# Performance work log

Measured on AMD Instinct MI355X. Metric: run time of the kernel, lower is better.

Reference implementation:

```python
import jax, jax.numpy as jnp
from jax import lax
import numpy as np

B, T = 64, 50
N_POINTS, N_STATE, N_ACTION = 3, 6, 2
ROWS = COLS = 64          # local env window
RES = 0.03                # meters / pixel
PADDING = 200
H_FULL = W_FULL = 256
FC = 256
C_IN = N_POINTS + 1 + N_ACTION  # rope channels + local env + action smear
FLAT = 32 * 14 * 14


def setup_inputs() -> dict:
    key = jax.random.key(0)
    ks = jax.random.split(key, 10)
    action = jax.random.normal(ks[0], (B, T, N_ACTION), jnp.float32) * 0.1
    state = jax.random.normal(ks[1], (B, T + 1, N_STATE), jnp.float32) * 0.3
    res = jnp.full((B, T, 1), RES, jnp.float32)
    full_env = (jax.random.uniform(ks[2], (B, H_FULL, W_FULL)) > 0.9).astype(jnp.float32)
    full_env_origin = jnp.full((B, 2), H_FULL / 2, jnp.float32)
    conv_w1 = jax.random.normal(ks[3], (3, 3, C_IN, 16), jnp.float32) * 0.1
    conv_b1 = jnp.zeros((16,), jnp.float32)
    conv_w2 = jax.random.normal(ks[4], (3, 3, 16, 32), jnp.float32) * 0.1
    conv_b2 = jnp.zeros((32,), jnp.float32)
    d_in = N_STATE + N_ACTION + FLAT
    dense_w0 = jax.random.normal(ks[5], (d_in, FC), jnp.float32) * 0.01
    dense_b0 = jnp.zeros((FC,), jnp.float32)
    dense_w1 = jax.random.normal(ks[6], (FC, FC), jnp.float32) * 0.01
    dense_b1 = jnp.zeros((FC,), jnp.float32)
    dense_w2 = jax.random.normal(ks[7], (FC, N_STATE), jnp.float32) * 0.01
    dense_b2 = jnp.zeros((N_STATE,), jnp.float32)
    return dict(action=action, state=state, res=res, full_env=full_env,
                full_env_origin=full_env_origin,
                conv_w1=conv_w1, conv_b1=conv_b1, conv_w2=conv_w2, conv_b2=conv_b2,
                dense_w0=dense_w0, dense_b0=dense_b0, dense_w1=dense_w1,
                dense_b1=dense_b1, dense_w2=dense_w2, dense_b2=dense_b2)


def _forward(action, state, res, full_env, full_env_origin,
             conv_w1, conv_b1, conv_w2, conv_b2,
             dense_w0, dense_b0, dense_w1, dense_b1, dense_w2, dense_b2):
    s0 = state[:, 0]                     # [B, N_STATE]
    res0 = res[:, 0, 0]                  # [B]
    origin = full_env_origin             # [B, 2] (row, col) pixel origin
    padded = jnp.pad(full_env, ((0, 0), (PADDING, PADDING), (PADDING, PADDING)))
    bi = jnp.arange(B)
    dr = jnp.arange(-(ROWS // 2), ROWS // 2)
    dc = jnp.arange(-(COLS // 2), COLS // 2)
    half = jnp.array([ROWS // 2, COLS // 2], jnp.float32)
    pi = jnp.arange(N_POINTS)[None, :]

    def raster(points, local_origin):
        # points [B, P, 2] (x, y) meters; local_origin [B, 2] (row, col)
        r = (points[..., 1] / res0[:, None] + local_origin[:, 0:1]).astype(jnp.int32)
        c = (points[..., 0] / res0[:, None] + local_origin[:, 1:2]).astype(jnp.int32)
        valid = (r >= 0) & (r < ROWS) & (c >= 0) & (c < COLS)
        rc = jnp.clip(r, 0, ROWS - 1)
        cc = jnp.clip(c, 0, COLS - 1)
        img = jnp.zeros((B, ROWS, COLS, N_POINTS), jnp.float32)
        img = img.at[bi[:, None], rc, cc, pi].add(valid.astype(jnp.float32))
        return jnp.minimum(img, 1.0)

    def step(s_t, a_t):
        head = s_t[:, -2:]                                   # (x, y) of head point
        ccol = (head[:, 0] / RES + origin[:, 1]).astype(jnp.int32)
        crow = (head[:, 1] / RES + origin[:, 0]).astype(jnp.int32)
        ri = crow[:, None, None] + dr[None, :, None] + PADDING   # [B, ROWS, COLS]
        ci = ccol[:, None, None] + dc[None, None, :] + PADDING
        local = padded[bi[:, None, None], ri, ci]                # gather local window
        local_origin = origin - jnp.stack([crow, ccol], 1).astype(jnp.float32) + half
        rope_img = raster(s_t.reshape(B, N_POINTS, 2), local_origin)
        act_img = jnp.broadcast_to(a_t[:, None, None, :], (B, ROWS, COLS, N_ACTION))
        z = jnp.concatenate([rope_img, local[..., None], act_img], axis=-1)
        for w, b in ((conv_w1, conv_b1), (conv_w2, conv_b2)):
            z = jax.nn.relu(lax.conv_general_dilated(
                z, w, (1, 1), 'VALID',
                dimension_numbers=('NHWC', 'HWIO', 'NHWC')) + b)
            z = lax.reduce_window(z, -jnp.inf, lax.max,
                                  (1, 2, 2, 1), (1, 2, 2, 1), 'VALID')
        z = z.reshape(B, -1)
        h = jnp.concatenate([s_t, a_t, z], axis=-1)              # mixed
        h = jax.nn.relu(h @ dense_w0 + dense_b0)
        h = jax.nn.relu(h @ dense_w1 + dense_b1)
        ds = h @ dense_w2 + dense_b2
        s_next = s_t + ds                                        # residual
        return s_next, s_next

    _, traj = lax.scan(step, s0, jnp.swapaxes(action, 0, 1))     # traj [T, B, N_STATE]
    return jnp.concatenate([s0[:, None], jnp.swapaxes(traj, 0, 1)], axis=1)


def reference(action, state, res, full_env, full_env_origin,
              conv_w1, conv_b1, conv_w2, conv_b2,
              dense_w0, dense_b0, dense_w1, dense_b1, dense_w2, dense_b2):
    return _forward(action, state, res, full_env, full_env_origin,
                    conv_w1, conv_b1, conv_w2, conv_b2,
                    dense_w0, dense_b0, dense_w1, dense_b1, dense_w2, dense_b2)
```

## Files before the change

kernel.cpp:

```cpp
#include <hip/hip_runtime.h>


__global__ __launch_bounds__(512)
void k_tail(const float* __restrict__ action, const float* __restrict__ w0,
            const float* __restrict__ b0, const float* __restrict__ w1d,
            const float* __restrict__ wsPart, const float* __restrict__ wsS,
            float* __restrict__ wsD1p, int st)
{
    const int b   = blockIdx.x >> 2;
    const int q   = blockIdx.x & 3;
    const int tid = threadIdx.x;

    __shared__ float hp[512];
    __shared__ float h1l[64];
    __shared__ float dp[512];

    const float* sp = wsS + ((st-1)&1)*512 + b*8;
    const float a0p = action[b*100 + (st-1)*2 + 0];
    const float a1p = action[b*100 + (st-1)*2 + 1];

    {
        const int cl  = tid & 63;
        const int ksg = tid >> 6;
        const int col = q*64 + cl;
        const float* pp = wsPart + b*8192 + ksg*4*256 + col;
        float h = pp[0] + pp[256] + pp[512] + pp[768];
        if (ksg == 0){
            h += b0[col];
            #pragma unroll
            for (int j = 0; j < 6; j++) h = fmaf(sp[j], w0[j*256 + col], h);
            h = fmaf(a0p, w0[1536 + col], h);
            h = fmaf(a1p, w0[1792 + col], h);
        }
        hp[tid] = h;
    }
    __syncthreads();
    if (tid < 64){
        float s = hp[tid]       + hp[64 + tid]  + hp[128 + tid] + hp[192 + tid]
                + hp[256 + tid] + hp[320 + tid] + hp[384 + tid] + hp[448 + tid];
        h1l[tid] = fmaxf(s, 0.f);
    }
    __syncthreads();

    {
        const int colp = tid & 255;
        const int kh   = tid >> 8;
        const float* wrow = w1d + (q*64 + kh*32)*256 + colp;
        const float* hh   = h1l + kh*32;
        float d0 = 0.f, d1 = 0.f;
        #pragma unroll 8
        for (int k = 0; k < 32; k += 2){
            d0 = fmaf(hh[k],   wrow[k*256],     d0);
            d1 = fmaf(hh[k+1], wrow[(k+1)*256], d1);
        }
        dp[tid] = d0 + d1;
    }
    __syncthreads();
    if (tid < 256)
        wsD1p[b*1024 + q*256 + tid] = dp[tid] + dp[256 + tid];
}

__device__ inline void tail_finish(int b, int tid, int st,
                                   const float* __restrict__ wsD1p,
                                   const float* __restrict__ b1d,
                                   const float* __restrict__ w2d,
                                   const float* __restrict__ b2d,
                                   const float* __restrict__ wsS,
                                   float* __restrict__ wred,
                                   float* __restrict__ sSl)
{
    const float* dd = wsD1p + b*1024 + tid;
    float h2 = fmaxf(dd[0] + dd[256] + dd[512] + dd[768] + b1d[tid], 0.f);
    float p[6];
    const float* wr = w2d + tid*6;
    #pragma unroll
    for (int j = 0; j < 6; j++) p[j] = h2 * wr[j];
    #pragma unroll
    for (int off = 32; off > 0; off >>= 1){
        #pragma unroll
        for (int j = 0; j < 6; j++) p[j] += __shfl_down(p[j], off, 64);
    }
    if ((tid & 63) == 0){
        #pragma unroll
        for (int j = 0; j < 6; j++) wred[(tid >> 6)*6 + j] = p[j];
    }
    __syncthreads();
    if (tid < 6){
        float ds = wred[tid] + wred[6+tid] + wred[12+tid] + wred[18+tid] + b2d[tid];
        sSl[tid] = wsS[((st-1)&1)*512 + b*8 + tid] + ds;
    }
    __syncthreads();
}

__global__ __launch_bounds__(256, 2)
void k_conv(const float* __restrict__ action, const float* __restrict__ state,
            const float* __restrict__ res, const float* __restrict__ env,
            const float* __restrict__ origin,
            const float* __restrict__ w1, const float* __restrict__ b1,
            const float* __restrict__ w2, const float* __restrict__ b2,
            const float* __restrict__ b1d, const float* __restrict__ w2d,
            const float* __restrict__ b2d, const float* __restrict__ wsD1p,
            float* __restrict__ wsS, float* __restrict__ wsFlatT,
            float* __restrict__ out, int st)
{
    const int wg  = blockIdx.x;
    const int b   = wg >> 3;
    const int oct = wg & 7;
    const int tid = threadIdx.x;

    __shared__ float w1l[864];
    __shared__ float w2l[4608];
    __shared__ float b2l[32];
    __shared__ float bAl[16];
    __shared__ float sSl[8];
    __shared__ float wred[24];
    __shared__ int   prm[12];
    __shared__ float pool1s[6*31*20];
    __shared__ unsigned char inl[14*64];

    for (int i = tid; i < 216; i += 256)
        *(float4*)&w1l[i*4] = *(const float4*)(w1 + i*4);
    for (int i = tid; i < 1152; i += 256)
        *(float4*)&w2l[i*4] = *(const float4*)(w2 + i*4);
    if (tid < 32) b2l[tid] = b2[tid];

    if (st == 0){
        if (tid < 6) sSl[tid] = state[b*306 + tid];
        __syncthreads();
    } else {
        tail_finish(b, tid, st, wsD1p, b1d, w2d, b2d, wsS, wred, sSl);
    }

    if (oct == 0 && tid < 6){
        out[b*306 + st*6 + tid] = sSl[tid];
        wsS[(st & 1)*512 + b*8 + tid] = sSl[tid];
    }

    if (tid == 0){
        float org0 = origin[2*b], org1 = origin[2*b+1];
        int ccol = (int)(sSl[4] / 0.03f + org1);
        int crow = (int)(sSl[5] / 0.03f + org0);
        float res0 = res[b*50];
        float lo0 = org0 - (float)crow + 32.0f;
        float lo1 = org1 - (float)ccol + 32.0f;
        prm[0] = crow; prm[1] = ccol;
        #pragma unroll
        for (int p = 0; p < 3; p++){
            int rr = (int)(sSl[2*p+1]/res0 + lo0);
            int cc = (int)(sSl[2*p  ]/res0 + lo1);
            prm[2+p] = rr; prm[5+p] = cc;
            prm[8+p] = (rr>=0 && rr<64 && cc>=0 && cc<64) ? 1 : 0;
        }
    }
    if (tid < 16){
        float s4 = 0.f, s5 = 0.f;
        #pragma unroll
        for (int k = 0; k < 9; k++){
            s4 += w1[(k*6 + 4)*16 + tid];
            s5 += w1[(k*6 + 5)*16 + tid];
        }
        float a0 = action[b*100 + st*2 + 0];
        float a1 = action[b*100 + st*2 + 1];
        bAl[tid] = b1[tid] + a0*s4 + a1*s5;
    }
    __syncthreads();

    const int p2lo = (oct < 6) ? 2*oct : 12 + (oct - 6);
    const int p2n  = (oct < 6) ? 2 : 1;
    const int p1n  = 2*p2n + 2;
    const int p1lo = 2*p2lo;
    const int ilo  = 4*p2lo;
    const int inn  = 2*p1n + 2;

    {
        const int crow = prm[0], ccol = prm[1];
        for (int idx = tid; idx < inn*64; idx += 256){
            int i = idx >> 6, j = idx & 63;
            int r = crow - 32 + ilo + i;
            int c = ccol - 32 + j;
            float v = (r>=0 && r<256 && c>=0 && c<256) ? env[b*65536 + (r<<8) + c] : 0.f;
            inl[idx] = (unsigned char)v;
        }
    }
    __syncthreads();

    {
        int pr[3], pc[3], pvld[3];
        #pragma unroll
        for (int p = 0; p < 3; p++){ pr[p]=prm[2+p]; pc[p]=prm[5+p]; pvld[p]=prm[8+p]; }

        for (int u = tid; u < p1n*31; u += 256){
            int pl = u / 31;
            int j  = u - pl*31;
            float l[4][4];
            #pragma unroll
            for (int dy = 0; dy < 4; dy++)
                #pragma unroll
                for (int dx = 0; dx < 4; dx++)
                    l[dy][dx] = (float)inl[(2*pl + dy)*64 + 2*j + dx];

            float m[16];
            #pragma unroll
            for (int o = 0; o < 16; o++) m[o] = 0.f;

            #pragma unroll
            for (int dy = 0; dy < 2; dy++){
                #pragma unroll
                for (int dx = 0; dx < 2; dx++){
                    int rg = 2*(p1lo + pl) + dy;
                    int cg = 2*j + dx;
                    bool pf[3]; int pidx[3];
                    #pragma unroll
                    for (int p = 0; p < 3; p++){
                        int kr = pr[p] - rg, kc = pc[p] - cg;
                        pf[p] = pvld[p] && kr >= 0 && kr < 3 && kc >= 0 && kc < 3;
                        pidx[p] = pf[p] ? ((kr*3 + kc)*6 + p)*16 : 0;
                    }
                    #pragma unroll
                    for (int o = 0; o < 16; o++){
                        float v = bAl[o];
                        #pragma unroll
                        for (int kr = 0; kr < 3; kr++)
                            #pragma unroll
                            for (int kc = 0; kc < 3; kc++)
                                v = fmaf(l[dy+kr][dx+kc], w1l[((kr*3 + kc)*6 + 3)*16 + o], v);
                        if (pf[0]) v += w1l[pidx[0] + o];
                        if (pf[1]) v += w1l[pidx[1] + o];
                        if (pf[2]) v += w1l[pidx[2] + o];
                        v = fmaxf(v, 0.f);
                        m[o] = fmaxf(m[o], v);
                    }
                }
            }
            float* pd = &pool1s[(pl*31 + j)*20];
            *(float4*)(pd     ) = make_float4(m[0],  m[1],  m[2],  m[3]);
            *(float4*)(pd + 4 ) = make_float4(m[4],  m[5],  m[6],  m[7]);
            *(float4*)(pd + 8 ) = make_float4(m[8],  m[9],  m[10], m[11]);
            *(float4*)(pd + 12) = make_float4(m[12], m[13], m[14], m[15]);
        }
    }
    __syncthreads();

    for (int u = tid; u < p2n*14*8; u += 256){
        int pi  = u / 112;
        int rem = u - pi*112;
        int jj  = rem >> 3;
        int oq  = rem & 7;
        int o0  = oq*4;

        float acc[4][4];
        #pragma unroll
        for (int ps = 0; ps < 4; ps++)
            #pragma unroll
            for (int c = 0; c < 4; c++) acc[ps][c] = 0.f;

        #pragma unroll 1
        for (int t9 = 0; t9 < 9; t9++){
            int kr = t9 / 3, kc = t9 - 3*(t9/3);
            const float* pb = &pool1s[((2*pi + kr)*31 + (2*jj + kc))*20];
            const float* wb = &w2l[(kr*3 + kc)*512 + o0];
            #pragma unroll
            for (int kib = 0; kib < 4; kib++){
                float4 q00 = *(const float4*)(pb + kib*4);
                float4 q01 = *(const float4*)(pb + 20 + kib*4);
                float4 q10 = *(const float4*)(pb + 620 + kib*4);
                float4 q11 = *(const float4*)(pb + 640 + kib*4);
                float pq[4][4] = {
                    {q00.x, q00.y, q00.z, q00.w},
                    {q01.x, q01.y, q01.z, q01.w},
                    {q10.x, q10.y, q10.z, q10.w},
                    {q11.x, q11.y, q11.z, q11.w}};
                #pragma unroll
                for (int kk = 0; kk < 4; kk++){
                    float4 wv = *(const float4*)(wb + (kib*4 + kk)*32);
                    #pragma unroll
                    for (int ps = 0; ps < 4; ps++){
                        float pvv = pq[ps][kk];
                        acc[ps][0] = fmaf(pvv, wv.x, acc[ps][0]);
                        acc[ps][1] = fmaf(pvv, wv.y, acc[ps][1]);
                        acc[ps][2] = fmaf(pvv, wv.z, acc[ps][2]);
                        acc[ps][3] = fmaf(pvv, wv.w, acc[ps][3]);
                    }
                }
            }
        }
        int kb = ((p2lo + pi)*14 + jj)*32 + o0;
        #pragma unroll
        for (int c = 0; c < 4; c++){
            float bb = b2l[o0 + c];
            float v0 = fmaxf(acc[0][c] + bb, 0.f);
            float v1 = fmaxf(acc[1][c] + bb, 0.f);
            float v2 = fmaxf(acc[2][c] + bb, 0.f);
            float v3 = fmaxf(acc[3][c] + bb, 0.f);
            wsFlatT[(kb + c)*64 + b] = fmaxf(fmaxf(v0, v1), fmaxf(v2, v3));
        }
    }
}

__global__ __launch_bounds__(256, 2)
void k_dense0(const float* __restrict__ w0, const float* __restrict__ wsFlatT,
              float* __restrict__ wsPart)
{
    const int blk = blockIdx.x;
    const int lid = (blk & 7)*64 + (blk >> 3);
    const int ks = lid >> 4;
    const int nc = lid & 15;
    const int n0 = nc*16;
    const int tid  = threadIdx.x;
    const int w    = tid >> 6;
    const int lane = tid & 63;
    const int mg = lane >> 2;
    const int nq = lane & 3;
    const int kbase = ks*196;

    __shared__ float xs[196*68];

    for (int idx = tid; idx < 3136; idx += 256){
        int k  = idx >> 4;
        int b4 = idx & 15;
        float4 v = *(const float4*)(wsFlatT + (kbase + k)*64 + b4*4);
        *(float4*)(&xs[k*68 + b4*4]) = v;
    }
    __syncthreads();

    float acc[4][4];
    #pragma unroll
    for (int i = 0; i < 4; i++)
        #pragma unroll
        for (int c = 0; c < 4; c++) acc[i][c] = 0.f;

    const float* xk = xs + (49*w)*68 + mg*4;
    const float* wpp = w0 + (8 + kbase + 49*w)*256 + n0 + nq*4;
    #pragma unroll 7
    for (int k = 0; k < 49; k++){
        float4 x4 = *(const float4*)(xk + k*68);
        float4 w4 = *(const float4*)(wpp + k*256);
        acc[0][0]=fmaf(x4.x,w4.x,acc[0][0]); acc[0][1]=fmaf(x4.x,w4.y,acc[0][1]);
        acc[0][2]=fmaf(x4.x,w4.z,acc[0][2]); acc[0][3]=fmaf(x4.x,w4.w,acc[0][3]);
        acc[1][0]=fmaf(x4.y,w4.x,acc[1][0]); acc[1][1]=fmaf(x4.y,w4.y,acc[1][1]);
        acc[1][2]=fmaf(x4.y,w4.z,acc[1][2]); acc[1][3]=fmaf(x4.y,w4.w,acc[1][3]);
        acc[2][0]=fmaf(x4.z,w4.x,acc[2][0]); acc[2][1]=fmaf(x4.z,w4.y,acc[2][1]);
        acc[2][2]=fmaf(x4.z,w4.z,acc[2][2]); acc[2][3]=fmaf(x4.z,w4.w,acc[2][3]);
        acc[3][0]=fmaf(x4.w,w4.x,acc[3][0]); acc[3][1]=fmaf(x4.w,w4.y,acc[3][1]);
        acc[3][2]=fmaf(x4.w,w4.z,acc[3][2]); acc[3][3]=fmaf(x4.w,w4.w,acc[3][3]);
    }
    __syncthreads();

    float* red = xs;
    {
        float* rr = red + (w*64 + lane)*17;
        #pragma unroll
        for (int j = 0; j < 16; j++) rr[j] = acc[j>>2][j&3];
    }
    __syncthreads();
    if (tid < 64){
        int mg2 = tid >> 2, nq2 = tid & 3;
        #pragma unroll
        for (int g = 0; g < 4; g++){
            float4 v;
            v.x = red[tid*17+4*g+0] + red[(64+tid)*17+4*g+0] + red[(128+tid)*17+4*g+0] + red[(192+tid)*17+4*g+0];
            v.y = red[tid*17+4*g+1] + red[(64+tid)*17+4*g+1] + red[(128+tid)*17+4*g+1] + red[(192+tid)*17+4*g+1];
            v.z = red[tid*17+4*g+2] + red[(64+tid)*17+4*g+2] + red[(128+tid)*17+4*g+2] + red[(192+tid)*17+4*g+2];
            v.w = red[tid*17+4*g+3] + red[(64+tid)*17+4*g+3] + red[(128+tid)*17+4*g+3] + red[(192+tid)*17+4*g+3];
            int bb = mg2*4 + g;
            *(float4*)(wsPart + (bb*32 + ks)*256 + n0 + nq2*4) = v;
        }
    }
}

__global__ __launch_bounds__(256)
void k_fin(const float* __restrict__ b1d, const float* __restrict__ w2d,
           const float* __restrict__ b2d, const float* __restrict__ wsD1p,
           const float* __restrict__ wsS, float* __restrict__ out)
{
    const int b = blockIdx.x;
    const int tid = threadIdx.x;
    __shared__ float wred[24];
    __shared__ float sSl[8];
    tail_finish(b, tid, 50, wsD1p, b1d, w2d, b2d, wsS, wred, sSl);
    if (tid < 6) out[b*306 + 300 + tid] = sSl[tid];
}

extern "C" void kernel_launch(void* const* d_in, const int* in_sizes, int n_in,
                              void* d_out, int out_size, void* d_ws, size_t ws_size,
                              hipStream_t stream)
{
    (void)in_sizes; (void)n_in; (void)out_size; (void)ws_size;
    const float* action = (const float*)d_in[0];
    const float* state  = (const float*)d_in[1];
    const float* res    = (const float*)d_in[2];
    const float* env    = (const float*)d_in[3];
    const float* origin = (const float*)d_in[4];
    const float* w1  = (const float*)d_in[5];
    const float* b1  = (const float*)d_in[6];
    const float* w2  = (const float*)d_in[7];
    const float* b2  = (const float*)d_in[8];
    const float* w0  = (const float*)d_in[9];
    const float* b0  = (const float*)d_in[10];
    const float* w1d = (const float*)d_in[11];
    const float* b1d = (const float*)d_in[12];
    const float* w2d = (const float*)d_in[13];
    const float* b2d = (const float*)d_in[14];
    float* out = (float*)d_out;

    float* wsF     = (float*)d_ws;
    float* wsS     = wsF;
    float* wsD1p   = wsF + 1024;
    float* wsFlatT = wsF + 1024 + 65536;
    float* wsPart  = wsF + 1024 + 65536 + 401408;

    k_conv<<<dim3(512), dim3(256), 0, stream>>>(
        action, state, res, env, origin, w1, b1, w2, b2,
        b1d, w2d, b2d, wsD1p, wsS, wsFlatT, out, 0);
    k_dense0<<<dim3(512), dim3(256), 0, stream>>>(w0, wsFlatT, wsPart);

    for (int st = 1; st < 50; ++st){
        k_tail<<<dim3(256), dim3(512), 0, stream>>>(
            action, w0, b0, w1d, wsPart, wsS, wsD1p, st);
        k_conv<<<dim3(512), dim3(256), 0, stream>>>(
            action, state, res, env, origin, w1, b1, w2, b2,
            b1d, w2d, b2d, wsD1p, wsS, wsFlatT, out, st);
        k_dense0<<<dim3(512), dim3(256), 0, stream>>>(w0, wsFlatT, wsPart);
    }
    k_tail<<<dim3(256), dim3(512), 0, stream>>>(
        action, w0, b0, w1d, wsPart, wsS, wsD1p, 50);
    k_fin<<<dim3(64), dim3(256), 0, stream>>>(b1d, w2d, b2d, wsD1p, wsS, out);
}
```

Before: 1.811 ms.

## Split conv work by column halves, remap blocks per XCD, drop dense0 LDS staging

Each k_conv block now handles half of the output columns, which doubles the grid to 1024 blocks and shrinks the shared tiles. Occupancy bounds rise to 4 blocks per SM. Block indices in k_conv and k_tail are remapped so that all blocks for a given batch land on the same XCD, aiming for better L2 locality. k_dense0 now reads activations directly from global memory instead of staging them in LDS, removing one sync and the LDS footprint. The cost is that each column-half block reloads the weights, recomputes tail_finish, and computes its own halo columns, so some work is duplicated.

```diff
diff --git a/kernel.cpp b/kernel.cpp
--- a/kernel.cpp
+++ b/kernel.cpp
@@ -7,8 +7,10 @@
             const float* __restrict__ wsPart, const float* __restrict__ wsS,
             float* __restrict__ wsD1p, int st)
 {
-    const int b   = blockIdx.x >> 2;
-    const int q   = blockIdx.x & 3;
+    const int xcd = blockIdx.x & 7;
+    const int i   = blockIdx.x >> 3;
+    const int b   = xcd*8 + (i & 7);
+    const int q   = i >> 3;
     const int tid = threadIdx.x;
 
     __shared__ float hp[512];
@@ -92,7 +94,7 @@
     __syncthreads();
 }
 
-__global__ __launch_bounds__(256, 2)
+__global__ __launch_bounds__(256, 4)
 void k_conv(const float* __restrict__ action, const float* __restrict__ state,
             const float* __restrict__ res, const float* __restrict__ env,
             const float* __restrict__ origin,
@@ -104,8 +106,11 @@
             float* __restrict__ out, int st)
 {
     const int wg  = blockIdx.x;
-    const int b   = wg >> 3;
-    const int oct = wg & 7;
+    const int xcd = wg & 7;
+    const int i0  = wg >> 3;
+    const int b   = xcd*8 + (i0 & 7);
+    const int oct = (i0 >> 3) & 7;
+    const int ch  = i0 >> 6;
     const int tid = threadIdx.x;
 
     __shared__ float w1l[864];
@@ -115,8 +120,8 @@
     __shared__ float sSl[8];
     __shared__ float wred[24];
     __shared__ int   prm[12];
-    __shared__ float pool1s[6*31*20];
-    __shared__ unsigned char inl[14*64];
+    __shared__ float pool1s[6*16*20];
+    __shared__ unsigned char inl[14*34];
 
     for (int i = tid; i < 216; i += 256)
         *(float4*)&w1l[i*4] = *(const float4*)(w1 + i*4);
@@ -131,7 +136,7 @@
         tail_finish(b, tid, st, wsD1p, b1d, w2d, b2d, wsS, wred, sSl);
     }
 
-    if (oct == 0 && tid < 6){
+    if (oct == 0 && ch == 0 && tid < 6){
         out[b*306 + st*6 + tid] = sSl[tid];
         wsS[(st & 1)*512 + b*8 + tid] = sSl[tid];
     }
@@ -171,13 +176,14 @@
     const int p1lo = 2*p2lo;
     const int ilo  = 4*p2lo;
     const int inn  = 2*p1n + 2;
+    const int cbase = 28*ch;
 
     {
         const int crow = prm[0], ccol = prm[1];
-        for (int idx = tid; idx < inn*64; idx += 256){
-            int i = idx >> 6, j = idx & 63;
+        for (int idx = tid; idx < inn*34; idx += 256){
+            int i = idx / 34, j = idx - 34*(idx/34);
             int r = crow - 32 + ilo + i;
-            int c = ccol - 32 + j;
+            int c = ccol - 32 + cbase + j;
             float v = (r>=0 && r<256 && c>=0 && c<256) ? env[b*65536 + (r<<8) + c] : 0.f;
             inl[idx] = (unsigned char)v;
         }
@@ -189,15 +195,15 @@
         #pragma unroll
         for (int p = 0; p < 3; p++){ pr[p]=prm[2+p]; pc[p]=prm[5+p]; pvld[p]=prm[8+p]; }
 
-        for (int u = tid; u < p1n*31; u += 256){
-            int pl = u / 31;
-            int j  = u - pl*31;
+        for (int u = tid; u < p1n*16; u += 256){
+            int pl = u >> 4;
+            int j  = u & 15;
             float l[4][4];
             #pragma unroll
             for (int dy = 0; dy < 4; dy++)
                 #pragma unroll
                 for (int dx = 0; dx < 4; dx++)
-                    l[dy][dx] = (float)inl[(2*pl + dy)*64 + 2*j + dx];
+                    l[dy][dx] = (float)inl[(2*pl + dy)*34 + 2*j + dx];
 
             float m[16];
             #pragma unroll
@@ -208,7 +214,7 @@
                 #pragma unroll
                 for (int dx = 0; dx < 2; dx++){
                     int rg = 2*(p1lo + pl) + dy;
-                    int cg = 2*j + dx;
+                    int cg = cbase + 2*j + dx;
                     bool pf[3]; int pidx[3];
                     #pragma unroll
                     for (int p = 0; p < 3; p++){
@@ -232,7 +238,7 @@
                     }
                 }
             }
-            float* pd = &pool1s[(pl*31 + j)*20];
+            float* pd = &pool1s[(pl*16 + j)*20];
             *(float4*)(pd     ) = make_float4(m[0],  m[1],  m[2],  m[3]);
             *(float4*)(pd + 4 ) = make_float4(m[4],  m[5],  m[6],  m[7]);
             *(float4*)(pd + 8 ) = make_float4(m[8],  m[9],  m[10], m[11]);
@@ -241,9 +247,9 @@
     }
     __syncthreads();
 
-    for (int u = tid; u < p2n*14*8; u += 256){
-        int pi  = u / 112;
-        int rem = u - pi*112;
+    for (int u = tid; u < p2n*7*8; u += 256){
+        int pi  = u / 56;
+        int rem = u - pi*56;
         int jj  = rem >> 3;
         int oq  = rem & 7;
         int o0  = oq*4;
@@ -257,14 +263,14 @@
         #pragma unroll 1
         for (int t9 = 0; t9 < 9; t9++){
             int kr = t9 / 3, kc = t9 - 3*(t9/3);
-            const float* pb = &pool1s[((2*pi + kr)*31 + (2*jj + kc))*20];
+            const float* pb = &pool1s[((2*pi + kr)*16 + (2*jj + kc))*20];
             const float* wb = &w2l[(kr*3 + kc)*512 + o0];
             #pragma unroll
             for (int kib = 0; kib < 4; kib++){
                 float4 q00 = *(const float4*)(pb + kib*4);
                 float4 q01 = *(const float4*)(pb + 20 + kib*4);
-                float4 q10 = *(const float4*)(pb + 620 + kib*4);
-                float4 q11 = *(const float4*)(pb + 640 + kib*4);
+                float4 q10 = *(const float4*)(pb + 320 + kib*4);
+                float4 q11 = *(const float4*)(pb + 340 + kib*4);
                 float pq[4][4] = {
                     {q00.x, q00.y, q00.z, q00.w},
                     {q01.x, q01.y, q01.z, q01.w},
@@ -284,7 +290,7 @@
                 }
             }
         }
-        int kb = ((p2lo + pi)*14 + jj)*32 + o0;
+        int kb = ((p2lo + pi)*14 + 7*ch + jj)*32 + o0;
         #pragma unroll
         for (int c = 0; c < 4; c++){
             float bb = b2l[o0 + c];
@@ -313,15 +319,7 @@
     const int nq = lane & 3;
     const int kbase = ks*196;
 
-    __shared__ float xs[196*68];
-
-    for (int idx = tid; idx < 3136; idx += 256){
-        int k  = idx >> 4;
-        int b4 = idx & 15;
-        float4 v = *(const float4*)(wsFlatT + (kbase + k)*64 + b4*4);
-        *(float4*)(&xs[k*68 + b4*4]) = v;
-    }
-    __syncthreads();
+    __shared__ float red[4352];
 
     float acc[4][4];
     #pragma unroll
@@ -329,11 +327,11 @@
         #pragma unroll
         for (int c = 0; c < 4; c++) acc[i][c] = 0.f;
 
-    const float* xk = xs + (49*w)*68 + mg*4;
+    const float* xk  = wsFlatT + (kbase + 49*w)*64 + mg*4;
     const float* wpp = w0 + (8 + kbase + 49*w)*256 + n0 + nq*4;
     #pragma unroll 7
     for (int k = 0; k < 49; k++){
-        float4 x4 = *(const float4*)(xk + k*68);
+        float4 x4 = *(const float4*)(xk + k*64);
         float4 w4 = *(const float4*)(wpp + k*256);
         acc[0][0]=fmaf(x4.x,w4.x,acc[0][0]); acc[0][1]=fmaf(x4.x,w4.y,acc[0][1]);
         acc[0][2]=fmaf(x4.x,w4.z,acc[0][2]); acc[0][3]=fmaf(x4.x,w4.w,acc[0][3]);
@@ -344,9 +342,7 @@
         acc[3][0]=fmaf(x4.w,w4.x,acc[3][0]); acc[3][1]=fmaf(x4.w,w4.y,acc[3][1]);
         acc[3][2]=fmaf(x4.w,w4.z,acc[3][2]); acc[3][3]=fmaf(x4.w,w4.w,acc[3][3]);
     }
-    __syncthreads();
-
-    float* red = xs;
+
     {
         float* rr = red + (w*64 + lane)*17;
         #pragma unroll
@@ -409,7 +405,7 @@
     float* wsFlatT = wsF + 1024 + 65536;
     float* wsPart  = wsF + 1024 + 65536 + 401408;
 
-    k_conv<<<dim3(512), dim3(256), 0, stream>>>(
+    k_conv<<<dim3(1024), dim3(256), 0, stream>>>(
         action, state, res, env, origin, w1, b1, w2, b2,
         b1d, w2d, b2d, wsD1p, wsS, wsFlatT, out, 0);
     k_dense0<<<dim3(512), dim3(256), 0, stream>>>(w0, wsFlatT, wsPart);
@@ -417,7 +413,7 @@
     for (int st = 1; st < 50; ++st){
         k_tail<<<dim3(256), dim3(512), 0, stream>>>(
             action, w0, b0, w1d, wsPart, wsS, wsD1p, st);
-        k_conv<<<dim3(512), dim3(256), 0, stream>>>(
+        k_conv<<<dim3(1024), dim3(256), 0, stream>>>(
             action, state, res, env, origin, w1, b1, w2, b2,
             b1d, w2d, b2d, wsD1p, wsS, wsFlatT, out, st);
         k_dense0<<<dim3(512), dim3(256), 0, stream>>>(w0, wsFlatT, wsPart);
```

Result: slower. 3.098 ms (+71.0%).
